# Optimization experiments

Measured on AMD Instinct MI355X. Metric: run time of the kernel, lower is better.

The kernel has to match this reference:

```python
import jax, jax.numpy as jnp
import numpy as np

IN_FEATURES = 1024
OUT_FEATURES = 256
GRID_SIZE = 5
SPLINE_ORDER = 3
SCALE_BASE = 1.0
GRID_RANGE = (-1.0, 1.0)


def make_grid():
    h = (GRID_RANGE[1] - GRID_RANGE[0]) / GRID_SIZE
    g = jnp.arange(-SPLINE_ORDER, GRID_SIZE + SPLINE_ORDER + 1, dtype=jnp.float32) * h + GRID_RANGE[0]
    # (in_features, grid_size + 2*spline_order + 1) = (1024, 12)
    return jnp.broadcast_to(g[None, :], (IN_FEATURES, g.shape[0]))


def setup_inputs() -> dict:
    key = jax.random.key(0)
    k1, k2, k3 = jax.random.split(key, 3)
    batch = 16384
    x = jax.random.normal(k1, (batch, IN_FEATURES), dtype=jnp.float32)
    base_weight = jax.random.normal(k2, (OUT_FEATURES, IN_FEATURES), dtype=jnp.float32) * 0.03
    n_basis = GRID_SIZE + SPLINE_ORDER  # 8
    spline_weight = (jax.random.uniform(k3, (OUT_FEATURES, IN_FEATURES * n_basis), dtype=jnp.float32) - 0.5) * 0.1 / n_basis
    grid = make_grid()
    return {"x": x, "base_weight": base_weight, "spline_weight": spline_weight, "grid": grid}


def b_splines(x, grid):
    # x: (B, F) -> (B, F, grid_size + spline_order)
    xe = x[:, :, None]  # (B, F, 1)
    bases = ((xe >= grid[:, :-1]) & (xe < grid[:, 1:])).astype(x.dtype)
    for k in range(1, SPLINE_ORDER + 1):
        left = (xe - grid[:, : -(k + 1)]) / (grid[:, k:-1] - grid[:, : -(k + 1)])
        right = (grid[:, k + 1 :] - xe) / (grid[:, k + 1 :] - grid[:, 1:-k])
        bases = left * bases[:, :, :-1] + right * bases[:, :, 1:]
    return bases.reshape(x.shape[0], -1)  # (B, F*(grid_size+spline_order))


def reference(x, base_weight, spline_weight, grid):
    base_out = jax.nn.silu(x) @ (base_weight * SCALE_BASE).T  # (B, out)
    spline_basis = b_splines(x, grid)                          # (B, F*8)
    spline_out = spline_basis @ spline_weight.T                # (B, out)
    return base_out + spline_out
```

## Files before the change

### kernel.cpp

```cpp
#include <hip/hip_runtime.h>
#include <cstdint>
#include <cstddef>

typedef unsigned short u16;
typedef unsigned int   u32;
typedef unsigned long long u64;
typedef __attribute__((ext_vector_type(8))) short short8;
typedef __attribute__((ext_vector_type(4))) float f32x4;

#define M_ROWS 16384
#define N_COLS 256
#define IN_F   1024
#define K_SPL  8192
#define K_TOT  9216
#define NCHUNK 144
#define SPLITK 2
#define CPB    (NCHUNK / SPLITK)

__device__ __forceinline__ u32 f2bf1(float f) {
  u32 u = __float_as_uint(f);
  u += 0x7fffu + ((u >> 16) & 1u);
  return u >> 16;
}
__device__ __forceinline__ u32 pk2(float a, float b) {
  return f2bf1(a) | (f2bf1(b) << 16);
}
__device__ __forceinline__ float silu(float v) {
  return v * __builtin_amdgcn_rcpf(1.f + __expf(-v));
}

__device__ __forceinline__ uint4 basis8(float xv) {
  float u = fmaf(xv, 2.5f, 5.5f);
  int i0 = (int)u;
  float fr = u - (float)i0;
  float fr2 = fr * fr, fr3 = fr2 * fr;
  float om  = 1.f - fr;
  float om3 = om * om * om;
  float w0 = om3 * (1.f / 6.f);
  float w3 = fr3 * (1.f / 6.f);
  float w1 = fmaf(fr3, 0.5f, fmaf(fr2, -1.f, 2.f / 3.f));
  float w2 = fmaf(fr + fr2 - fr3, 0.5f, 1.f / 6.f);
  u64 W = (u64)pk2(w0, w1) | ((u64)pk2(w2, w3) << 32);
  if (!(u >= 0.f && u < 11.f)) W = 0ull;
  int s = (i0 - 3) * 16;
  u64 lo, hi;
  if (s >= 64)      { int r = s - 64; lo = 0ull; hi = (r < 64) ? (W << r) : 0ull; }
  else if (s > 0)   { lo = W << s;    hi = W >> (64 - s); }
  else if (s == 0)  { lo = W;         hi = 0ull; }
  else              { int r = -s;     lo = (r < 64) ? (W >> r) : 0ull; hi = 0ull; }
  uint4 o;
  o.x = (u32)lo; o.y = (u32)(lo >> 32); o.z = (u32)hi; o.w = (u32)(hi >> 32);
  return o;
}

__global__ void pack_weights(const float* __restrict__ bw, const float* __restrict__ sw,
                             u16* __restrict__ Bp) {
  int o  = blockIdx.y;
  int k4 = (blockIdx.x * blockDim.x + threadIdx.x) * 4;
  const float* src = (k4 < K_SPL) ? (sw + (size_t)o * K_SPL + k4)
                                  : (bw + (size_t)o * IN_F + (k4 - K_SPL));
  float a = src[0], b = src[1], c = src[2], d = src[3];
  uint2 v; v.x = pk2(a, b); v.y = pk2(c, d);
  *(uint2*)(Bp + (size_t)o * K_TOT + k4) = v;
}

__global__ __launch_bounds__(512, 4)
void kan_gemm(const float* __restrict__ x, const u16* __restrict__ Bp,
              float* __restrict__ out) {
  __shared__ __align__(16) u16 As[64 * 64];
  __shared__ __align__(16) u16 Bs[256 * 64];

  const int tid  = threadIdx.x;
  const int lane = tid & 63;
  const int w    = tid >> 6;
  const int wm   = w & 1;
  const int wn   = w >> 1;

  const int bid  = blockIdx.x;
  const int kid  = bid & 1;
  const int mb   = bid >> 1;
  const int row0 = mb * 64;
  const int cs   = kid * CPB, c1 = cs + CPB;

  f32x4 acc[2][4];
#pragma unroll
  for (int i = 0; i < 2; ++i)
#pragma unroll
    for (int j = 0; j < 4; ++j)
      acc[i][j] = (f32x4){0.f, 0.f, 0.f, 0.f};

  const int sr = tid >> 3;
  const int sq = tid & 7;

  const int lm = lane & 15;
  const int kg = lane >> 4;
  int a_off[2][2], b_off[2][4];
#pragma unroll
  for (int h = 0; h < 2; ++h) {
    int c = h * 4 + kg;
#pragma unroll
    for (int i = 0; i < 2; ++i) {
      int ra = wm * 32 + i * 16 + lm;
      a_off[h][i] = ra * 64 + ((c ^ (ra & 7)) * 8);
    }
#pragma unroll
    for (int j = 0; j < 4; ++j) {
      int rb = wn * 64 + j * 16 + lm;
      b_off[h][j] = rb * 64 + ((c ^ (rb & 7)) * 8);
    }
  }

  float px;
  float4 pb0, pb1;

  auto LOADX = [&](int c) {
    if (c < 128) {
      px = x[(size_t)(row0 + sr) * IN_F + c * 8 + sq];
    } else {
      const float* xp = x + (size_t)(row0 + sr) * IN_F + (c - 128) * 64 + sq * 8;
      pb0 = *(const float4*)xp;
      pb1 = *(const float4*)(xp + 4);
    }
  };

  auto BUILD = [&](int c) {
    uint4 q;
    if (c < 128) {
      q = basis8(px);
    } else {
      q.x = pk2(silu(pb0.x), silu(pb0.y));
      q.y = pk2(silu(pb0.z), silu(pb0.w));
      q.z = pk2(silu(pb1.x), silu(pb1.y));
      q.w = pk2(silu(pb1.z), silu(pb1.w));
    }
    *(uint4*)(As + sr * 64 + ((sq ^ (sr & 7)) * 8)) = q;
  };

  auto STAGEB = [&](int c) {
#pragma unroll
    for (int it = 0; it < 4; ++it) {
      int s = tid + it * 512;
      int r_ = s >> 3, cc = (s & 7) ^ (r_ & 7);
      const u16* gp = Bp + (size_t)r_ * K_TOT + c * 64 + cc * 8;
      __builtin_amdgcn_global_load_lds((const __attribute__((address_space(1))) void*)gp,
                                       (__attribute__((address_space(3))) void*)(Bs + s * 8),
                                       16, 0, 0);
    }
  };

  LOADX(cs);
  for (int c = cs; c < c1; ++c) {
    BUILD(c);
    STAGEB(c);
    if (c + 1 < c1) LOADX(c + 1);
    __syncthreads();
#pragma unroll
    for (int h = 0; h < 2; ++h) {
      short8 af[2], bf[4];
#pragma unroll
      for (int i = 0; i < 2; ++i) af[i] = *(const short8*)(As + a_off[h][i]);
#pragma unroll
      for (int j = 0; j < 4; ++j) bf[j] = *(const short8*)(Bs + b_off[h][j]);
#pragma unroll
      for (int i = 0; i < 2; ++i)
#pragma unroll
        for (int j = 0; j < 4; ++j)
          acc[i][j] = __builtin_amdgcn_mfma_f32_16x16x32_bf16(af[i], bf[j], acc[i][j], 0, 0, 0);
    }
    __syncthreads();
  }

  const int lc = lane & 15;
  const int lr = (lane >> 4) * 4;
#pragma unroll
  for (int i = 0; i < 2; ++i) {
#pragma unroll
    for (int j = 0; j < 4; ++j) {
      int gr = row0 + wm * 32 + i * 16 + lr;
      int gc = wn * 64 + j * 16 + lc;
      float* po = out + (size_t)gr * N_COLS + gc;
#pragma unroll
      for (int r = 0; r < 4; ++r)
        unsafeAtomicAdd(po + (size_t)r * N_COLS, acc[i][j][r]);
    }
  }
}

extern "C" void kernel_launch(void* const* d_in, const int* in_sizes, int n_in,
                              void* d_out, int out_size, void* d_ws, size_t ws_size,
                              hipStream_t stream) {
  const float* x  = (const float*)d_in[0];
  const float* bw = (const float*)d_in[1];
  const float* sw = (const float*)d_in[2];
  float* out = (float*)d_out;
  u16* Bp = (u16*)d_ws;

  hipMemsetAsync(d_out, 0, (size_t)M_ROWS * N_COLS * sizeof(float), stream);

  dim3 pgrid(K_TOT / 4 / 256, N_COLS);
  pack_weights<<<pgrid, 256, 0, stream>>>(bw, sw, Bp);

  kan_gemm<<<512, 512, 0, stream>>>(x, Bp, out);
}
```

Measured before the change: 213.2 us.

## Double-buffer LDS tiles, use 4 waves per block, fold output zeroing into pack kernel

The GEMM kernel now double-buffers the A and B shared-memory tiles, so the next chunk's B loads and basis/SiLU build are issued before the MFMAs on the current chunk, leaving one barrier per iteration. Each block drops from 8 waves to 4, and each wave covers all 64 rows and a 64-column slice, so MFMA work per wave doubles. The separate memset is removed and the output is zeroed inside pack_weights, saving a launch. In exchange, LDS per block doubles, occupancy per CU falls, and register pressure from 16 accumulators rises.

```diff
diff --git a/kernel.cpp b/kernel.cpp
--- a/kernel.cpp
+++ b/kernel.cpp
@@ -54,7 +54,7 @@
 }
 
 __global__ void pack_weights(const float* __restrict__ bw, const float* __restrict__ sw,
-                             u16* __restrict__ Bp) {
+                             u16* __restrict__ Bp, float* __restrict__ out) {
   int o  = blockIdx.y;
   int k4 = (blockIdx.x * blockDim.x + threadIdx.x) * 4;
   const float* src = (k4 < K_SPL) ? (sw + (size_t)o * K_SPL + k4)
@@ -62,19 +62,24 @@
   float a = src[0], b = src[1], c = src[2], d = src[3];
   uint2 v; v.x = pk2(a, b); v.y = pk2(c, d);
   *(uint2*)(Bp + (size_t)o * K_TOT + k4) = v;
-}
-
-__global__ __launch_bounds__(512, 4)
+
+  int flat = (blockIdx.y * gridDim.x + blockIdx.x) * blockDim.x + threadIdx.x;
+  if (flat < (M_ROWS * N_COLS / 8)) {
+    float4 z = {0.f, 0.f, 0.f, 0.f};
+    ((float4*)out)[flat * 2]     = z;
+    ((float4*)out)[flat * 2 + 1] = z;
+  }
+}
+
+__global__ __launch_bounds__(256, 2)
 void kan_gemm(const float* __restrict__ x, const u16* __restrict__ Bp,
               float* __restrict__ out) {
-  __shared__ __align__(16) u16 As[64 * 64];
-  __shared__ __align__(16) u16 Bs[256 * 64];
+  __shared__ __align__(16) u16 As[2][64 * 64];
+  __shared__ __align__(16) u16 Bs[2][256 * 64];
 
   const int tid  = threadIdx.x;
   const int lane = tid & 63;
   const int w    = tid >> 6;
-  const int wm   = w & 1;
-  const int wn   = w >> 1;
 
   const int bid  = blockIdx.x;
   const int kid  = bid & 1;
@@ -82,102 +87,123 @@
   const int row0 = mb * 64;
   const int cs   = kid * CPB, c1 = cs + CPB;
 
-  f32x4 acc[2][4];
-#pragma unroll
-  for (int i = 0; i < 2; ++i)
+  f32x4 acc[4][4];
+#pragma unroll
+  for (int i = 0; i < 4; ++i)
 #pragma unroll
     for (int j = 0; j < 4; ++j)
       acc[i][j] = (f32x4){0.f, 0.f, 0.f, 0.f};
 
-  const int sr = tid >> 3;
-  const int sq = tid & 7;
+  const int sr = tid >> 2;
+  const int sq = tid & 3;
 
   const int lm = lane & 15;
   const int kg = lane >> 4;
-  int a_off[2][2], b_off[2][4];
+  int a_off[2][4], b_off[2][4];
 #pragma unroll
   for (int h = 0; h < 2; ++h) {
     int c = h * 4 + kg;
 #pragma unroll
-    for (int i = 0; i < 2; ++i) {
-      int ra = wm * 32 + i * 16 + lm;
+    for (int i = 0; i < 4; ++i) {
+      int ra = i * 16 + lm;
       a_off[h][i] = ra * 64 + ((c ^ (ra & 7)) * 8);
     }
 #pragma unroll
     for (int j = 0; j < 4; ++j) {
-      int rb = wn * 64 + j * 16 + lm;
+      int rb = w * 64 + j * 16 + lm;
       b_off[h][j] = rb * 64 + ((c ^ (rb & 7)) * 8);
     }
   }
 
-  float px;
-  float4 pb0, pb1;
+  float px0, px1;
+  float4 pb0, pb1, pb2, pb3;
 
   auto LOADX = [&](int c) {
     if (c < 128) {
-      px = x[(size_t)(row0 + sr) * IN_F + c * 8 + sq];
+      const float* xp = x + (size_t)(row0 + sr) * IN_F + c * 8 + sq;
+      px0 = xp[0];
+      px1 = xp[4];
     } else {
-      const float* xp = x + (size_t)(row0 + sr) * IN_F + (c - 128) * 64 + sq * 8;
+      const float* xp = x + (size_t)(row0 + sr) * IN_F + (c - 128) * 64 + sq * 16;
       pb0 = *(const float4*)xp;
       pb1 = *(const float4*)(xp + 4);
+      pb2 = *(const float4*)(xp + 8);
+      pb3 = *(const float4*)(xp + 12);
     }
   };
 
-  auto BUILD = [&](int c) {
-    uint4 q;
+  auto BUILD = [&](int c, u16* A) {
     if (c < 128) {
-      q = basis8(px);
+      *(uint4*)(A + sr * 64 + ((sq ^ (sr & 7)) * 8))       = basis8(px0);
+      *(uint4*)(A + sr * 64 + (((sq + 4) ^ (sr & 7)) * 8)) = basis8(px1);
     } else {
-      q.x = pk2(silu(pb0.x), silu(pb0.y));
-      q.y = pk2(silu(pb0.z), silu(pb0.w));
-      q.z = pk2(silu(pb1.x), silu(pb1.y));
-      q.w = pk2(silu(pb1.z), silu(pb1.w));
-    }
-    *(uint4*)(As + sr * 64 + ((sq ^ (sr & 7)) * 8)) = q;
+      uint4 q0, q1;
+      q0.x = pk2(silu(pb0.x), silu(pb0.y));
+      q0.y = pk2(silu(pb0.z), silu(pb0.w));
+      q0.z = pk2(silu(pb1.x), silu(pb1.y));
+      q0.w = pk2(silu(pb1.z), silu(pb1.w));
+      q1.x = pk2(silu(pb2.x), silu(pb2.y));
+      q1.y = pk2(silu(pb2.z), silu(pb2.w));
+      q1.z = pk2(silu(pb3.x), silu(pb3.y));
+      q1.w = pk2(silu(pb3.z), silu(pb3.w));
+      int cc0 = sq * 2, cc1 = sq * 2 + 1;
+      *(uint4*)(A + sr * 64 + ((cc0 ^ (sr & 7)) * 8)) = q0;
+      *(uint4*)(A + sr * 64 + ((cc1 ^ (sr & 7)) * 8)) = q1;
+    }
   };
 
-  auto STAGEB = [&](int c) {
-#pragma unroll
-    for (int it = 0; it < 4; ++it) {
-      int s = tid + it * 512;
+  auto STAGEB = [&](int c, u16* B) {
+#pragma unroll
+    for (int it = 0; it < 8; ++it) {
+      int s = tid + it * 256;
       int r_ = s >> 3, cc = (s & 7) ^ (r_ & 7);
       const u16* gp = Bp + (size_t)r_ * K_TOT + c * 64 + cc * 8;
       __builtin_amdgcn_global_load_lds((const __attribute__((address_space(1))) void*)gp,
-                                       (__attribute__((address_space(3))) void*)(Bs + s * 8),
+                                       (__attribute__((address_space(3))) void*)(B + s * 8),
                                        16, 0, 0);
     }
   };
 
   LOADX(cs);
+  BUILD(cs, As[0]);
+  STAGEB(cs, Bs[0]);
+  LOADX(cs + 1);
+  __syncthreads();
+
+  int b = 0;
   for (int c = cs; c < c1; ++c) {
-    BUILD(c);
-    STAGEB(c);
-    if (c + 1 < c1) LOADX(c + 1);
-    __syncthreads();
+    if (c + 1 < c1) {
+      STAGEB(c + 1, Bs[b ^ 1]);
+      BUILD(c + 1, As[b ^ 1]);
+      if (c + 2 < c1) LOADX(c + 2);
+    }
+    const u16* Ab = As[b];
+    const u16* Bb = Bs[b];
 #pragma unroll
     for (int h = 0; h < 2; ++h) {
-      short8 af[2], bf[4];
-#pragma unroll
-      for (int i = 0; i < 2; ++i) af[i] = *(const short8*)(As + a_off[h][i]);
-#pragma unroll
-      for (int j = 0; j < 4; ++j) bf[j] = *(const short8*)(Bs + b_off[h][j]);
-#pragma unroll
-      for (int i = 0; i < 2; ++i)
+      short8 af[4], bf[4];
+#pragma unroll
+      for (int i = 0; i < 4; ++i) af[i] = *(const short8*)(Ab + a_off[h][i]);
+#pragma unroll
+      for (int j = 0; j < 4; ++j) bf[j] = *(const short8*)(Bb + b_off[h][j]);
+#pragma unroll
+      for (int i = 0; i < 4; ++i)
 #pragma unroll
         for (int j = 0; j < 4; ++j)
           acc[i][j] = __builtin_amdgcn_mfma_f32_16x16x32_bf16(af[i], bf[j], acc[i][j], 0, 0, 0);
     }
     __syncthreads();
+    b ^= 1;
   }
 
   const int lc = lane & 15;
   const int lr = (lane >> 4) * 4;
 #pragma unroll
-  for (int i = 0; i < 2; ++i) {
+  for (int i = 0; i < 4; ++i) {
 #pragma unroll
     for (int j = 0; j < 4; ++j) {
-      int gr = row0 + wm * 32 + i * 16 + lr;
-      int gc = wn * 64 + j * 16 + lc;
+      int gr = row0 + i * 16 + lr;
+      int gc = w * 64 + j * 16 + lc;
       float* po = out + (size_t)gr * N_COLS + gc;
 #pragma unroll
       for (int r = 0; r < 4; ++r)
@@ -195,10 +221,8 @@
   float* out = (float*)d_out;
   u16* Bp = (u16*)d_ws;
 
-  hipMemsetAsync(d_out, 0, (size_t)M_ROWS * N_COLS * sizeof(float), stream);
-
   dim3 pgrid(K_TOT / 4 / 256, N_COLS);
-  pack_weights<<<pgrid, 256, 0, stream>>>(bw, sw, Bp);
-
-  kan_gemm<<<512, 512, 0, stream>>>(x, Bp, out);
-}
+  pack_weights<<<pgrid, 256, 0, stream>>>(bw, sw, Bp, out);
+
+  kan_gemm<<<M_ROWS / 64 * SPLITK, 256, 0, stream>>>(x, Bp, out);
+}
```

After: 214.7 us. No clear change (+0.7%).
